# Kernel optimization log

Hardware: AMD Instinct MI355X
Metric: run time of the kernel (lower is better)

Reference implementation:

```python
import jax, jax.numpy as jnp
import numpy as np

B, S, IK, IV = 16, 2048, 3, 1
D = IK + IV          # input_size = 4
H = 256              # hidden_size
F = 512              # dim_feedforward
L = 2                # num_layers
EPS = 1e-5


def setup_inputs() -> dict:
    key = jax.random.key(0)
    ks = jax.random.split(key, 16)
    n = jax.random.normal
    inp = {
        'KEY': n(ks[0], (B, S, IK), jnp.float32),
        'VALUE': n(ks[1], (B, S, IV), jnp.float32),
        # per-layer kernel-attention projections (stacked on layer axis)
        'Wq': n(ks[2], (L, D, H), jnp.float32) * 0.1,
        'bq': jnp.zeros((L, H), jnp.float32),
        'Wk': n(ks[3], (L, D, H), jnp.float32) * 0.1,
        'bk': jnp.zeros((L, H), jnp.float32),
        'Wv': n(ks[4], (L, D, H), jnp.float32) * 0.1,
        'bv': jnp.zeros((L, H), jnp.float32),
        'Wo': n(ks[5], (L, H, D), jnp.float32) * 0.1,
        'bo': jnp.zeros((L, D), jnp.float32),
        'bw': jnp.ones((L,), jnp.float32),          # Gaussian kernel bandwidth
        # LayerNorm 1
        'g1': jnp.ones((L, D), jnp.float32),
        'be1': jnp.zeros((L, D), jnp.float32),
        # FFN
        'W1': n(ks[6], (L, D, F), jnp.float32) * 0.1,
        'b1': jnp.zeros((L, F), jnp.float32),
        'W2': n(ks[7], (L, F, D), jnp.float32) * 0.1,
        'b2': jnp.zeros((L, D), jnp.float32),
        # LayerNorm 2
        'g2': jnp.ones((L, D), jnp.float32),
        'be2': jnp.zeros((L, D), jnp.float32),
        # final fc: input_size -> input_v
        'Wfc': n(ks[8], (D, IV), jnp.float32) * 0.1,
        'bfc': jnp.zeros((IV,), jnp.float32),
    }
    return inp


def _layernorm(x, g, b):
    m = x.mean(-1, keepdims=True)
    v = ((x - m) ** 2).mean(-1, keepdims=True)
    return (x - m) * jax.lax.rsqrt(v + EPS) * g + b


def reference(KEY, VALUE, Wq, bq, Wk, bk, Wv, bv, Wo, bo, bw,
              g1, be1, W1, b1, W2, b2, g2, be2, Wfc, bfc):
    # positioning: concat coords and values -> [B, S, D]
    X = jnp.concatenate([KEY, VALUE], axis=-1)
    n_layers = Wq.shape[0]
    for i in range(n_layers):
        # Nadaraya-Watson Gaussian kernel attention (madsnn, type='nwd', kernel='gauss')
        Q = X @ Wq[i] + bq[i]                      # [B,S,H]
        K = X @ Wk[i] + bk[i]                      # [B,S,H]
        V = X @ Wv[i] + bv[i]                      # [B,S,H]
        # pairwise squared distances ||q-k||^2, [B,S,S]
        d2 = ((Q * Q).sum(-1)[:, :, None]
              + (K * K).sum(-1)[:, None, :]
              - 2.0 * jnp.einsum('bqh,bkh->bqk', Q, K))
        attn = jax.nn.softmax(-0.5 * d2 * (bw[i] ** 2), axis=-1)
        attn_out = jnp.einsum('bqk,bkh->bqh', attn, V) @ Wo[i] + bo[i]  # [B,S,D]
        # residual + LayerNorm + FFN + residual + LayerNorm (dropout = identity in eval)
        res = _layernorm(X + attn_out, g1[i], be1[i])
        ff = jax.nn.relu(res @ W1[i] + b1[i]) @ W2[i] + b2[i]
        X = _layernorm(res + ff, g2[i], be2[i])
    return X @ Wfc + bfc                            # [B,S,IV]
```

## Files before the change

kernel.cpp:

```cpp
#include <hip/hip_runtime.h>

#define BB 16
#define SS 2048
#define NTOK (BB*SS)
#define FF 512
#define EPSF 1e-5f

#if __has_builtin(__builtin_amdgcn_exp2f)
#define EXP2F(x) __builtin_amdgcn_exp2f(x)
#else
#define EXP2F(x) exp2f(x)
#endif


__device__ __forceinline__ float wred64(float v) {
#pragma unroll
  for (int m = 32; m > 0; m >>= 1) v += __shfl_xor(v, m, 64);
  return v;
}


__global__ __launch_bounds__(64) void prep_kernel(
    const float* __restrict__ Wq, const float* __restrict__ bq,
    const float* __restrict__ Wk, const float* __restrict__ bk,
    const float* __restrict__ Wv, const float* __restrict__ bv,
    const float* __restrict__ Wo, const float* __restrict__ bw,
    const float* __restrict__ W1, const float* __restrict__ b1,
    const float* __restrict__ W2,
    float* __restrict__ sm, float* __restrict__ w1t)
{
  const int i = blockIdx.x;
  const int lane = threadIdx.x;
  float m4[4][4] = {{0}}, gkk[4][4] = {{0}}, wvo[4][4] = {{0}};
  float akk[4] = {0}, bvo[4] = {0};
  float ck1 = 0.f, ck2 = 0.f;

  for (int h = lane; h < 256; h += 64) {
    float vq[4], vk[4], vv[4], wo4[4];
#pragma unroll
    for (int a = 0; a < 4; ++a) {
      vq[a]  = Wq[(i*4 + a)*256 + h];
      vk[a]  = Wk[(i*4 + a)*256 + h];
      vv[a]  = Wv[(i*4 + a)*256 + h];
      wo4[a] = Wo[(i*256 + h)*4 + a];
    }
    const float bqh = bq[i*256 + h], bkh = bk[i*256 + h], bvh = bv[i*256 + h];
#pragma unroll
    for (int a = 0; a < 4; ++a) {
#pragma unroll
      for (int c = 0; c < 4; ++c) {
        m4[a][c]  = fmaf(vq[a], vk[c], m4[a][c]);
        gkk[a][c] = fmaf(vk[a], vk[c], gkk[a][c]);
        wvo[a][c] = fmaf(vv[a], wo4[c], wvo[a][c]);
      }
      akk[a] = fmaf(vk[a], bqh - bkh, akk[a]);
      bvo[a] = fmaf(bvh, wo4[a], bvo[a]);
    }
    ck1 = fmaf(bqh, bkh, ck1);
    ck2 = fmaf(bkh, bkh, ck2);
  }
#pragma unroll
  for (int a = 0; a < 4; ++a) {
#pragma unroll
    for (int c = 0; c < 4; ++c) {
      m4[a][c]  = wred64(m4[a][c]);
      gkk[a][c] = wred64(gkk[a][c]);
      wvo[a][c] = wred64(wvo[a][c]);
    }
    akk[a] = wred64(akk[a]);
    bvo[a] = wred64(bvo[a]);
  }
  ck1 = wred64(ck1); ck2 = wred64(ck2);

  if (lane == 0) {
    const float bwv = bw[i];
    const float bw2 = bwv * bwv * 1.44269504088896f;
    float* s = sm + i*64;
#pragma unroll
    for (int a = 0; a < 4; ++a) {
#pragma unroll
      for (int c = 0; c < 4; ++c) {
        s[a*4+c]      = bw2 * m4[a][c];
        s[16 + a*4+c] = -0.5f * bw2 * gkk[a][c];
        s[32 + a*4+c] = wvo[a][c];
      }
      s[48+a] = bw2 * akk[a];
      s[52+a] = bvo[a];
    }
    s[56] = bw2 * (ck1 - 0.5f * ck2);
  }
  for (int f = lane; f < FF; f += 64) {
    float* rec = w1t + (i*FF + f)*12;
#pragma unroll
    for (int c = 0; c < 4; ++c) rec[c]   = W1[(i*4 + c)*FF + f];
#pragma unroll
    for (int c = 0; c < 4; ++c) rec[4+c] = W2[(i*FF + f)*4 + c];
    rec[8] = b1[i*FF + f];
    rec[9] = 0.f; rec[10] = 0.f; rec[11] = 0.f;
  }
}

__device__ __forceinline__ void compute_feat(const float x[4], const float* __restrict__ s,
                                             float* __restrict__ featrec)
{
  float P[4], VT[4], tk[4];
#pragma unroll
  for (int a = 0; a < 4; ++a) {
    P[a]  = fmaf(s[a*4+3], x[3], fmaf(s[a*4+2], x[2], fmaf(s[a*4+1], x[1], s[a*4+0]*x[0])));
    tk[a] = fmaf(s[16+a*4+3], x[3], fmaf(s[16+a*4+2], x[2], fmaf(s[16+a*4+1], x[1], s[16+a*4+0]*x[0])));
    VT[a] = s[52+a] + fmaf(s[32+3*4+a], x[3], fmaf(s[32+2*4+a], x[2], fmaf(s[32+1*4+a], x[1], s[32+0*4+a]*x[0])));
  }
  float R = s[56];
#pragma unroll
  for (int a = 0; a < 4; ++a) R = fmaf(tk[a] + s[48+a], x[a], R);
  float4* fp = (float4*)featrec;
  fp[0] = make_float4(P[0], P[1], P[2], P[3]);
  fp[1] = make_float4(VT[0], VT[1], VT[2], VT[3]);
  fp[2] = make_float4(R, 0.f, 0.f, 0.f);
}

__global__ __launch_bounds__(256) void f0_kernel(
    const float* __restrict__ KEY, const float* __restrict__ VALUE,
    const float* __restrict__ sm, float* __restrict__ X0, float* __restrict__ feat)
{
  const int gq = blockIdx.x*256 + threadIdx.x;
  float x[4];
  x[0] = KEY[gq*3 + 0];
  x[1] = KEY[gq*3 + 1];
  x[2] = KEY[gq*3 + 2];
  x[3] = VALUE[gq];
  *(float4*)(X0 + (size_t)gq*4) = make_float4(x[0], x[1], x[2], x[3]);
  float fr[12];
  compute_feat(x, sm, fr);
  float4* fp = (float4*)(feat + (size_t)gq*12);
  fp[0] = ((float4*)fr)[0]; fp[1] = ((float4*)fr)[1]; fp[2] = ((float4*)fr)[2];
}

__global__ __launch_bounds__(256) void attn_kernel(
    const float* __restrict__ feat, const float* __restrict__ X,
    float* __restrict__ part)
{
  __shared__ float kbuf[256*12];
  const int bid = blockIdx.x;
  const int b = bid >> 5;
  const int r = bid & 31;
  const int qg = r >> 3, kb = r & 7;
  const int qbase = (b << 11) + (qg << 9);
  const int kbase = (b << 11) + (kb << 8);
  const int tid = threadIdx.x;
  const int lane = tid & 63, wave = tid >> 6;

  {
    const float4* src = (const float4*)(feat + (size_t)kbase*12);
    float4* dst = (float4*)kbuf;
    dst[tid] = src[tid];
    dst[tid + 256] = src[tid + 256];
    dst[tid + 512] = src[tid + 512];
  }

  float xq[8][4], acc[8][5];
#pragma unroll
  for (int j = 0; j < 8; ++j) {
    const float4 xv = *(const float4*)(X + (size_t)(qbase + j*64 + lane)*4);
    xq[j][0] = xv.x; xq[j][1] = xv.y; xq[j][2] = xv.z; xq[j][3] = xv.w;
#pragma unroll
    for (int c = 0; c < 5; ++c) acc[j][c] = 0.f;
  }
  __syncthreads();

  const float* kf = kbuf + wave*64*12;
#pragma unroll 2
  for (int k = 0; k < 64; ++k) {
    const float* kp = kf + k*12;
    const float4 P  = *(const float4*)kp;
    const float4 VT = *(const float4*)(kp + 4);
    const float R = kp[8];
#pragma unroll
    for (int j = 0; j < 8; ++j) {
      float l = fmaf(xq[j][3], P.w, fmaf(xq[j][2], P.z,
                fmaf(xq[j][1], P.y, fmaf(xq[j][0], P.x, R))));
      const float e = EXP2F(l);
      acc[j][0] = fmaf(e, VT.x, acc[j][0]);
      acc[j][1] = fmaf(e, VT.y, acc[j][1]);
      acc[j][2] = fmaf(e, VT.z, acc[j][2]);
      acc[j][3] = fmaf(e, VT.w, acc[j][3]);
      acc[j][4] += e;
    }
  }

  const int stripe = (kb << 2) + wave;
  float* pb = part + (size_t)stripe * NTOK * 5;
#pragma unroll
  for (int j = 0; j < 8; ++j) {
    float* pp = pb + (size_t)(qbase + j*64 + lane)*5;
    pp[0] = acc[j][0]; pp[1] = acc[j][1]; pp[2] = acc[j][2];
    pp[3] = acc[j][3]; pp[4] = acc[j][4];
  }
}

__device__ __forceinline__ void ln4(const float t[4], const float* __restrict__ g,
                                    const float* __restrict__ b, float r[4])
{
  const float m = 0.25f*(t[0]+t[1]+t[2]+t[3]);
  const float d0 = t[0]-m, d1 = t[1]-m, d2 = t[2]-m, d3 = t[3]-m;
  const float v = 0.25f*(d0*d0 + d1*d1 + d2*d2 + d3*d3);
  const float sc = rsqrtf(v + EPSF);
  r[0] = fmaf(d0*sc, g[0], b[0]);
  r[1] = fmaf(d1*sc, g[1], b[1]);
  r[2] = fmaf(d2*sc, g[2], b[2]);
  r[3] = fmaf(d3*sc, g[3], b[3]);
}

__global__ __launch_bounds__(512) void combine_kernel(
    const float* __restrict__ part, const float* __restrict__ Xin,
    const float* __restrict__ w1t,
    const float* __restrict__ bo, const float* __restrict__ g1, const float* __restrict__ be1,
    const float* __restrict__ b2v, const float* __restrict__ g2, const float* __restrict__ be2,
    const float* __restrict__ smn,
    float* __restrict__ Xout, float* __restrict__ feat,
    const float* __restrict__ Wfc, const float* __restrict__ bfc,
    float* __restrict__ outp, int last)
{
  const int tok = threadIdx.x & 63, fc = threadIdx.x >> 6;
  const int gq = blockIdx.x*64 + tok;
  __shared__ float redp[8][64][5];
  __shared__ float ress[64][4];
  __shared__ float redf[8][64][4];

  {
    float a5[5] = {0,0,0,0,0};
#pragma unroll
    for (int s = 0; s < 4; ++s) {
      const float* pp = part + ((size_t)(fc*4 + s)*NTOK + gq)*5;
#pragma unroll
      for (int c = 0; c < 5; ++c) a5[c] += pp[c];
    }
#pragma unroll
    for (int c = 0; c < 5; ++c) redp[fc][tok][c] = a5[c];
  }
  __syncthreads();

  if (fc == 0) {
    float acc[5] = {0,0,0,0,0};
#pragma unroll
    for (int k = 0; k < 8; ++k)
#pragma unroll
      for (int c = 0; c < 5; ++c) acc[c] += redp[k][tok][c];
    const float inv = 1.0f / acc[4];
    const float4 xv = *(const float4*)(Xin + (size_t)gq*4);
    float t[4];
    t[0] = xv.x + fmaf(acc[0], inv, bo[0]);
    t[1] = xv.y + fmaf(acc[1], inv, bo[1]);
    t[2] = xv.z + fmaf(acc[2], inv, bo[2]);
    t[3] = xv.w + fmaf(acc[3], inv, bo[3]);
    float r[4];
    ln4(t, g1, be1, r);
    ress[tok][0] = r[0]; ress[tok][1] = r[1]; ress[tok][2] = r[2]; ress[tok][3] = r[3];
  }
  __syncthreads();

  const float r0 = ress[tok][0], r1 = ress[tok][1], r2 = ress[tok][2], r3 = ress[tok][3];
  float fa[4] = {0,0,0,0};
  const float* wt = w1t + (size_t)fc*64*12;
#pragma unroll 4
  for (int f = 0; f < 64; ++f) {
    const float* rec = wt + f*12;
    const float4 w1r = *(const float4*)rec;
    const float4 w2r = *(const float4*)(rec + 4);
    const float b1f = rec[8];
    float h = fmaf(r3, w1r.w, fmaf(r2, w1r.z, fmaf(r1, w1r.y, fmaf(r0, w1r.x, b1f))));
    h = fmaxf(h, 0.f);
    fa[0] = fmaf(h, w2r.x, fa[0]);
    fa[1] = fmaf(h, w2r.y, fa[1]);
    fa[2] = fmaf(h, w2r.z, fa[2]);
    fa[3] = fmaf(h, w2r.w, fa[3]);
  }
  redf[fc][tok][0] = fa[0]; redf[fc][tok][1] = fa[1];
  redf[fc][tok][2] = fa[2]; redf[fc][tok][3] = fa[3];
  __syncthreads();

  if (fc == 0) {
    float t2[4];
#pragma unroll
    for (int c = 0; c < 4; ++c) {
      float s = b2v[c];
#pragma unroll
      for (int k = 0; k < 8; ++k) s += redf[k][tok][c];
      t2[c] = ress[tok][c] + s;
    }
    float y[4];
    ln4(t2, g2, be2, y);
    if (last) {
      outp[gq] = fmaf(y[3], Wfc[3], fmaf(y[2], Wfc[2], fmaf(y[1], Wfc[1], fmaf(y[0], Wfc[0], bfc[0]))));
    } else {
      *(float4*)(Xout + (size_t)gq*4) = make_float4(y[0], y[1], y[2], y[3]);
      float fr[12];
      compute_feat(y, smn, fr);
      float4* fp = (float4*)(feat + (size_t)gq*12);
      fp[0] = ((float4*)fr)[0]; fp[1] = ((float4*)fr)[1]; fp[2] = ((float4*)fr)[2];
    }
  }
}

extern "C" void kernel_launch(void* const* d_in, const int* in_sizes, int n_in,
                              void* d_out, int out_size, void* d_ws, size_t ws_size,
                              hipStream_t stream)
{
  const float* KEY   = (const float*)d_in[0];
  const float* VALUE = (const float*)d_in[1];
  const float* Wq  = (const float*)d_in[2];
  const float* bq  = (const float*)d_in[3];
  const float* Wk  = (const float*)d_in[4];
  const float* bk  = (const float*)d_in[5];
  const float* Wv  = (const float*)d_in[6];
  const float* bv  = (const float*)d_in[7];
  const float* Wo  = (const float*)d_in[8];
  const float* bo  = (const float*)d_in[9];
  const float* bw  = (const float*)d_in[10];
  const float* g1  = (const float*)d_in[11];
  const float* be1 = (const float*)d_in[12];
  const float* W1  = (const float*)d_in[13];
  const float* b1  = (const float*)d_in[14];
  const float* W2  = (const float*)d_in[15];
  const float* b2  = (const float*)d_in[16];
  const float* g2  = (const float*)d_in[17];
  const float* be2 = (const float*)d_in[18];
  const float* Wfc = (const float*)d_in[19];
  const float* bfc = (const float*)d_in[20];
  float* out = (float*)d_out;

  float* w    = (float*)d_ws;
  float* sm   = w;
  float* w1t  = w + 128;
  float* feat = w + 12416;
  float* X0   = w + 405632;
  float* X1   = w + 536704;
  float* part = w + 667776;

  prep_kernel<<<2, 64, 0, stream>>>(Wq, bq, Wk, bk, Wv, bv, Wo, bw, W1, b1, W2, sm, w1t);
  f0_kernel<<<128, 256, 0, stream>>>(KEY, VALUE, sm, X0, feat);

  attn_kernel<<<512, 256, 0, stream>>>(feat, X0, part);
  combine_kernel<<<512, 512, 0, stream>>>(part, X0, w1t,
      bo, g1, be1, b2, g2, be2,
      sm + 64, X1, feat, Wfc, bfc, out, 0);

  attn_kernel<<<512, 256, 0, stream>>>(feat, X1, part);
  combine_kernel<<<512, 512, 0, stream>>>(part, X1, w1t + FF*12,
      bo + 4, g1 + 4, be1 + 4, b2 + 4, g2 + 4, be2 + 4,
      sm, X0, feat, Wfc, bfc, out, 1);
}
```

Measured before the change: 198.4 us.

## Reduce per-wave attention partials in LDS before writing to global

New measurement: 191.8 us. -3.3%, faster.

```diff
diff --git a/kernel.cpp b/kernel.cpp
--- a/kernel.cpp
+++ b/kernel.cpp
@@ -140,7 +140,7 @@
     const float* __restrict__ feat, const float* __restrict__ X,
     float* __restrict__ part)
 {
-  __shared__ float kbuf[256*12];
+  __shared__ float smem[512*21];
   const int bid = blockIdx.x;
   const int b = bid >> 5;
   const int r = bid & 31;
@@ -152,7 +152,7 @@
 
   {
     const float4* src = (const float4*)(feat + (size_t)kbase*12);
-    float4* dst = (float4*)kbuf;
+    float4* dst = (float4*)smem;
     dst[tid] = src[tid];
     dst[tid + 256] = src[tid + 256];
     dst[tid + 512] = src[tid + 512];
@@ -168,7 +168,7 @@
   }
   __syncthreads();
 
-  const float* kf = kbuf + wave*64*12;
+  const float* kf = smem + wave*64*12;
 #pragma unroll 2
   for (int k = 0; k < 64; ++k) {
     const float* kp = kf + k*12;
@@ -187,14 +187,28 @@
       acc[j][4] += e;
     }
   }
-
-  const int stripe = (kb << 2) + wave;
-  float* pb = part + (size_t)stripe * NTOK * 5;
+  __syncthreads();
 #pragma unroll
   for (int j = 0; j < 8; ++j) {
-    float* pp = pb + (size_t)(qbase + j*64 + lane)*5;
-    pp[0] = acc[j][0]; pp[1] = acc[j][1]; pp[2] = acc[j][2];
-    pp[3] = acc[j][3]; pp[4] = acc[j][4];
+    float* rr = smem + (j*64 + lane)*21 + wave*5;
+    rr[0] = acc[j][0]; rr[1] = acc[j][1]; rr[2] = acc[j][2];
+    rr[3] = acc[j][3]; rr[4] = acc[j][4];
+  }
+  __syncthreads();
+  float* pb = part + (size_t)kb * NTOK * 8;
+#pragma unroll
+  for (int t = 0; t < 2; ++t) {
+    const int q = t*256 + tid;
+    const float* rr = smem + q*21;
+    float s0 = 0.f, s1 = 0.f, s2 = 0.f, s3 = 0.f, s4 = 0.f;
+#pragma unroll
+    for (int w = 0; w < 4; ++w) {
+      s0 += rr[w*5+0]; s1 += rr[w*5+1]; s2 += rr[w*5+2];
+      s3 += rr[w*5+3]; s4 += rr[w*5+4];
+    }
+    float* pp = pb + (size_t)(qbase + q)*8;
+    *(float4*)pp = make_float4(s0, s1, s2, s3);
+    pp[4] = s4;
   }
 }
 
@@ -228,15 +242,11 @@
   __shared__ float redf[8][64][4];
 
   {
-    float a5[5] = {0,0,0,0,0};
-#pragma unroll
-    for (int s = 0; s < 4; ++s) {
-      const float* pp = part + ((size_t)(fc*4 + s)*NTOK + gq)*5;
-#pragma unroll
-      for (int c = 0; c < 5; ++c) a5[c] += pp[c];
-    }
-#pragma unroll
-    for (int c = 0; c < 5; ++c) redp[fc][tok][c] = a5[c];
+    const float* pp = part + ((size_t)fc*NTOK + gq)*8;
+    const float4 v = *(const float4*)pp;
+    redp[fc][tok][0] = v.x; redp[fc][tok][1] = v.y;
+    redp[fc][tok][2] = v.z; redp[fc][tok][3] = v.w;
+    redp[fc][tok][4] = pp[4];
   }
   __syncthreads();
 
```
